# Kernel tuning notes

Measured on AMD Instinct MI355X. Metric: run time of the kernel, lower is better.

The kernel has to match this reference:

```python
import jax, jax.numpy as jnp
import numpy as np

N_POINTS = 262144
SP_FEAT = 128
HIDDEN = 64
EMBED = 256
NUM_SP = 4096
NUM_SP2 = 256
PAD_LIMIT = 64
MASK_RATIO = 0.6


def setup_inputs() -> dict:
    key = jax.random.key(0)
    ks = jax.random.split(key, 6)
    x = jax.random.normal(ks[0], (N_POINTS, SP_FEAT), jnp.float32)
    # point -> superpoint ids, sorted; force every superpoint non-empty
    idx10 = jax.random.randint(ks[1], (N_POINTS,), 0, NUM_SP)
    idx10 = jnp.sort(idx10.at[:NUM_SP].set(jnp.arange(NUM_SP))).astype(jnp.int32)
    # superpoint -> higher superpoint, balanced (16 per group, < PAD_LIMIT), sorted
    idx21 = ((jnp.arange(NUM_SP) * NUM_SP2) // NUM_SP).astype(jnp.int32)
    # deterministic mask: exactly int(NUM_SP * MASK_RATIO) superpoints masked
    mask_num = int(NUM_SP * MASK_RATIO)
    perm = jax.random.permutation(ks[2], NUM_SP)
    is_masked = jnp.zeros((NUM_SP,), bool).at[perm[:mask_num]].set(True)
    W1 = jax.random.normal(ks[3], (SP_FEAT, HIDDEN), jnp.float32) / np.sqrt(SP_FEAT).astype(np.float32)
    b1 = jnp.zeros((HIDDEN,), jnp.float32)
    W2 = jax.random.normal(ks[4], (HIDDEN, EMBED), jnp.float32) / np.sqrt(HIDDEN).astype(np.float32)
    b2 = jnp.zeros((EMBED,), jnp.float32)
    return {
        "full_features": x,
        "full_super_indices_10": idx10,
        "full_super_indices_21": idx21,
        "is_masked": is_masked,
        "W1": W1, "b1": b1, "W2": W2, "b2": b2,
    }


def _pad_scatter(tokens, idx21, flag):
    # tokens: [NUM_SP, C]; idx21 sorted sp->sp2 ids; flag: [NUM_SP] bool.
    # rank of each flagged superpoint within its sp2 group (in sp order)
    f = flag.astype(jnp.int32)
    cum = jnp.cumsum(f)                                            # inclusive global cumsum
    per_group = jax.ops.segment_sum(f, idx21, num_segments=NUM_SP2)
    prefix = jnp.concatenate([jnp.zeros((1,), jnp.int32), jnp.cumsum(per_group)[:-1]])
    rank = cum - 1 - prefix[idx21]                                 # 0-based slot within group
    slot = jnp.where(flag, rank, PAD_LIMIT)                        # PAD_LIMIT -> dropped
    out = jnp.zeros((NUM_SP2, PAD_LIMIT, tokens.shape[-1]), tokens.dtype)
    return out.at[idx21, slot].set(tokens, mode="drop")


def reference(full_features, full_super_indices_10, full_super_indices_21,
              is_masked, W1, b1, W2, b2):
    # per-point 2-layer MLP (gather is implicit: MLP is pointwise), then segment max
    h = jax.nn.relu(full_features @ W1 + b1)                       # [N, HIDDEN]
    h = jax.nn.relu(h @ W2 + b2)                                   # [N, EMBED]
    tok = jax.ops.segment_max(h, full_super_indices_10, num_segments=NUM_SP)  # [NUM_SP, EMBED]
    remain_tokens = _pad_scatter(tok, full_super_indices_21, ~is_masked)      # [NUM_SP2, PAD, EMBED]
    mask_tokens = _pad_scatter(tok, full_super_indices_21, is_masked)         # [NUM_SP2, PAD, EMBED]
    return (remain_tokens, mask_tokens)
```

## Files before the change

kernel.cpp:

```cpp
#include <hip/hip_runtime.h>
#include <hip/hip_bf16.h>

#define N_POINTS 262144
#define SP_FEAT 128
#define HIDDEN 64
#define EMBED 256
#define NUM_SP 4096
#define NUM_SP2 256
#define PAD_LIMIT 64
#define SLOTS 4
#define XS_STRIDE 136
#define H1_STRIDE 76
#define LOCAL_SP 4

typedef __bf16 bf16x8 __attribute__((ext_vector_type(8)));
typedef float floatx4 __attribute__((ext_vector_type(4)));
using bf16 = __hip_bfloat16;

__global__ __launch_bounds__(256) void fused_prep_kernel(
    const float* __restrict__ W1, const float* __restrict__ W2,
    const int* __restrict__ idx10, const int* __restrict__ idx21,
    const void* __restrict__ is_masked,
    bf16* __restrict__ W1t, bf16* __restrict__ W2t,
    int* __restrict__ start, int* __restrict__ invR, int* __restrict__ invM)
{
    const int tid = threadIdx.x;
    const int blk = blockIdx.x;

    if (blk < 256) {
        int p0 = (blk * 256 + tid) * 4;
        int4 v = *(const int4*)(idx10 + p0);
        if (p0 == 0) { start[0] = 0; start[NUM_SP] = N_POINTS; }
        if (v.y != v.x) start[v.y] = p0 + 1;
        if (v.z != v.y) start[v.z] = p0 + 2;
        if (v.w != v.z) start[v.w] = p0 + 3;
        if (p0 + 4 < N_POINTS) {
            int nx = idx10[p0 + 4];
            if (nx != v.w) start[nx] = p0 + 4;
        }
        return;
    }
    if (blk < 352) {
        int i = (blk - 256) * 256 + tid;
        if (i < HIDDEN * SP_FEAT) {
            int n = i >> 7, k = i & 127;
            W1t[i] = __float2bfloat16(W1[k * HIDDEN + n]);
        } else {
            int j = i - HIDDEN * SP_FEAT;
            int n = j >> 6, k = j & 63;
            W2t[j] = __float2bfloat16(W2[k * EMBED + n]);
        }
        return;
    }
    __shared__ int encS;
    if (tid == 0) encS = 0;
    __syncthreads();
    const unsigned char* mb = (const unsigned char*)is_masked;
    const int* mi = (const int*)is_masked;
    int local = 0;
    for (int p = tid; p < NUM_SP; p += 256)
        if ((p & 3) && mb[p]) local = 1;
    if (local) atomicOr(&encS, 1);
    __syncthreads();
    const int e = encS;

    const int g = tid;
    int a = 0, b = NUM_SP;
    while (a < b) { int m = (a + b) >> 1; if (idx21[m] < g) a = m + 1; else b = m; }
    int lo = a;
    b = NUM_SP;
    while (a < b) { int m = (a + b) >> 1; if (idx21[m] < g + 1) a = m + 1; else b = m; }
    int hi = a;
    int nR = 0, nM = 0;
    for (int s = lo; s < hi; ++s) {
        int msk = e ? (int)mb[s] : mi[s];
        if (msk) { if (nM < PAD_LIMIT) invM[g * PAD_LIMIT + nM] = s; nM++; }
        else     { if (nR < PAD_LIMIT) invR[g * PAD_LIMIT + nR] = s; nR++; }
    }
    for (int r = nR; r < PAD_LIMIT; ++r) invR[g * PAD_LIMIT + r] = -1;
    for (int r = nM; r < PAD_LIMIT; ++r) invM[g * PAD_LIMIT + r] = -1;
}

__global__ __launch_bounds__(256, 4) void mlp_segmax_kernel(
    const float* __restrict__ X, const int* __restrict__ idx10,
    const int* __restrict__ start,
    const bf16* __restrict__ W1t, const float* __restrict__ b1,
    const bf16* __restrict__ W2t, const float* __restrict__ b2,
    float* __restrict__ partial)
{
    __shared__ __align__(16) bf16 Xs[64][XS_STRIDE];
    __shared__ __align__(16) bf16 H1s[64][H1_STRIDE];
    __shared__ int tokL[LOCAL_SP][EMBED];
    __shared__ int sIdx[64];

    const int tid  = threadIdx.x;
    const int lane = tid & 63;
    const int w    = tid >> 6;
    const int l15  = lane & 15;
    const int quad = lane >> 4;
    const int b    = blockIdx.x;
    const int m0   = b * 64;

    float4 u0[4], u1[4];
#pragma unroll
    for (int i = 0; i < 4; ++i) {
        int c   = tid + 256 * i;
        int row = c >> 4;
        int cc  = (c & 15) * 8;
        const float* src = X + (size_t)(m0 + row) * SP_FEAT + cc;
        u0[i] = *(const float4*)src;
        u1[i] = *(const float4*)(src + 4);
    }
    if (tid < 64) sIdx[tid] = idx10[m0 + tid];
#pragma unroll
    for (int j = 0; j < LOCAL_SP; ++j) tokL[j][tid] = 0;

    bf16x8 bw1[4];
    {
        const bf16* p = W1t + (16 * w + l15) * SP_FEAT + quad * 8;
#pragma unroll
        for (int ks = 0; ks < 4; ++ks) bw1[ks] = *(const bf16x8*)(p + 32 * ks);
    }
    const float b1v = b1[16 * w + l15];

    __builtin_amdgcn_sched_barrier(0);

#pragma unroll
    for (int i = 0; i < 4; ++i) {
        int c   = tid + 256 * i;
        int row = c >> 4;
        int cc  = (c & 15) * 8;
        union { bf16x8 v; bf16 h[8]; } u;
        u.h[0] = __float2bfloat16(u0[i].x); u.h[1] = __float2bfloat16(u0[i].y);
        u.h[2] = __float2bfloat16(u0[i].z); u.h[3] = __float2bfloat16(u0[i].w);
        u.h[4] = __float2bfloat16(u1[i].x); u.h[5] = __float2bfloat16(u1[i].y);
        u.h[6] = __float2bfloat16(u1[i].z); u.h[7] = __float2bfloat16(u1[i].w);
        *(bf16x8*)(&Xs[row][cc]) = u.v;
    }
    __syncthreads();

    floatx4 zero4 = {0.f, 0.f, 0.f, 0.f};
    floatx4 acc1[4] = {zero4, zero4, zero4, zero4};
#pragma unroll
    for (int ks = 0; ks < 4; ++ks) {
        int k = ks * 32 + quad * 8;
#pragma unroll
        for (int tm = 0; tm < 4; ++tm) {
            bf16x8 a = *(bf16x8*)(&Xs[16 * tm + l15][k]);
            acc1[tm] = __builtin_amdgcn_mfma_f32_16x16x32_bf16(a, bw1[ks], acc1[tm], 0, 0, 0);
        }
    }
#pragma unroll
    for (int tm = 0; tm < 4; ++tm) {
#pragma unroll
        for (int r = 0; r < 4; ++r) {
            float v = acc1[tm][r] + b1v;
            v = v > 0.f ? v : 0.f;
            H1s[16 * tm + quad * 4 + r][16 * w + l15] = __float2bfloat16(v);
        }
    }
    __syncthreads();

    bf16x8 bf2[4][2];
#pragma unroll
    for (int tn = 0; tn < 4; ++tn) {
        const bf16* p = W2t + (64 * w + 16 * tn + l15) * HIDDEN + quad * 8;
#pragma unroll
        for (int ks = 0; ks < 2; ++ks) bf2[tn][ks] = *(const bf16x8*)(p + 32 * ks);
    }
    float b2f[4];
#pragma unroll
    for (int tn = 0; tn < 4; ++tn) b2f[tn] = b2[64 * w + 16 * tn + l15];

    bf16x8 afr[4][2];
    int sps[16];
#pragma unroll
    for (int tm = 0; tm < 4; ++tm) {
        afr[tm][0] = *(bf16x8*)(&H1s[16 * tm + l15][quad * 8]);
        afr[tm][1] = *(bf16x8*)(&H1s[16 * tm + l15][32 + quad * 8]);
        int4 s4 = *(const int4*)(&sIdx[16 * tm + 4 * quad]);
        sps[4 * tm + 0] = s4.x; sps[4 * tm + 1] = s4.y;
        sps[4 * tm + 2] = s4.z; sps[4 * tm + 3] = s4.w;
    }
    const int sp0 = sIdx[0];

#pragma unroll
    for (int tn = 0; tn < 4; ++tn) {
        const int col = 64 * w + 16 * tn + l15;
        int cur_sp = -1;
        float cur = 0.f;
#pragma unroll
        for (int tm = 0; tm < 4; ++tm) {
            floatx4 acc = zero4;
            acc = __builtin_amdgcn_mfma_f32_16x16x32_bf16(afr[tm][0], bf2[tn][0], acc, 0, 0, 0);
            acc = __builtin_amdgcn_mfma_f32_16x16x32_bf16(afr[tm][1], bf2[tn][1], acc, 0, 0, 0);
#pragma unroll
            for (int r = 0; r < 4; ++r) {
                float v = acc[r] + b2f[tn];
                v = v > 0.f ? v : 0.f;
                int sp = sps[4 * tm + r];
                if (sp == cur_sp) {
                    cur = fmaxf(cur, v);
                } else {
                    if (cur_sp >= 0) {
                        int local = cur_sp - sp0;
                        if (local < LOCAL_SP) {
                            atomicMax(&tokL[local][col], __float_as_int(cur));
                        } else {
                            int slot = b - (start[cur_sp] >> 6);
                            atomicMax((int*)(partial + ((size_t)cur_sp * SLOTS +
                                      (slot < 3 ? slot : 3)) * EMBED + col),
                                      __float_as_int(cur));
                        }
                    }
                    cur_sp = sp;
                    cur = v;
                }
            }
        }
        {
            int local = cur_sp - sp0;
            if (local < LOCAL_SP) {
                atomicMax(&tokL[local][col], __float_as_int(cur));
            } else {
                int slot = b - (start[cur_sp] >> 6);
                atomicMax((int*)(partial + ((size_t)cur_sp * SLOTS +
                          (slot < 3 ? slot : 3)) * EMBED + col),
                          __float_as_int(cur));
            }
        }
    }
    __syncthreads();

    int nsp = sIdx[63] - sp0 + 1;
    if (nsp > LOCAL_SP) nsp = LOCAL_SP;
    for (int j = 0; j < nsp; ++j) {
        int sp   = sp0 + j;
        int slot = b - (start[sp] >> 6);
        int bits = tokL[j][tid];
        int* dst = (int*)(partial + ((size_t)sp * SLOTS + (slot < 3 ? slot : 3)) * EMBED + tid);
        if (slot < 3) *dst = bits;
        else atomicMax(dst, bits);
    }
}

__global__ __launch_bounds__(256) void scatter_kernel(
    const float4* __restrict__ partial4, const int* __restrict__ start,
    const int* __restrict__ invR, const int* __restrict__ invM,
    float4* __restrict__ out4)
{
    const int bb   = blockIdx.x;
    const int g    = bb & (NUM_SP2 - 1);
    const int slab = bb >> 8;
    const int tid  = threadIdx.x;
    const int c4   = tid & 63;
    const int r0   = tid >> 6;
    const int* tab = slab ? invM : invR;
    float4* o = out4 + ((size_t)slab * NUM_SP2 + g) * PAD_LIMIT * 64;
#pragma unroll 4
    for (int rr = 0; rr < 16; ++rr) {
        int row = r0 + rr * 4;
        int sp = tab[g * PAD_LIMIT + row];
        float4 v = {0.f, 0.f, 0.f, 0.f};
        if (sp >= 0) {
            int sb = start[sp] >> 6;
            int se = (start[sp + 1] - 1) >> 6;
            int ns = se - sb;
            const float4* p = partial4 + (size_t)sp * SLOTS * 64 + c4;
            v = p[0];
            if (ns > 0) {
                float4 q = p[64];
                v.x = fmaxf(v.x, q.x); v.y = fmaxf(v.y, q.y);
                v.z = fmaxf(v.z, q.z); v.w = fmaxf(v.w, q.w);
            }
            if (ns > 1) {
                float4 q = p[128];
                v.x = fmaxf(v.x, q.x); v.y = fmaxf(v.y, q.y);
                v.z = fmaxf(v.z, q.z); v.w = fmaxf(v.w, q.w);
            }
            if (ns > 2) {
                float4 q = p[192];
                v.x = fmaxf(v.x, q.x); v.y = fmaxf(v.y, q.y);
                v.z = fmaxf(v.z, q.z); v.w = fmaxf(v.w, q.w);
            }
        }
        o[row * 64 + c4] = v;
    }
}

extern "C" void kernel_launch(void* const* d_in, const int* in_sizes, int n_in,
                              void* d_out, int out_size, void* d_ws, size_t ws_size,
                              hipStream_t stream) {
    (void)in_sizes; (void)n_in; (void)ws_size; (void)out_size;
    const float* X        = (const float*)d_in[0];
    const int* idx10      = (const int*)d_in[1];
    const int* idx21      = (const int*)d_in[2];
    const void* is_masked = (const void*)d_in[3];
    const float* W1       = (const float*)d_in[4];
    const float* b1       = (const float*)d_in[5];
    const float* W2       = (const float*)d_in[6];
    const float* b2       = (const float*)d_in[7];

    char* ws       = (char*)d_ws;
    float* partial = (float*)ws;
    bf16* W1t      = (bf16*)(ws + (size_t)NUM_SP * SLOTS * EMBED * 4);
    bf16* W2t      = W1t + HIDDEN * SP_FEAT;
    int*  start    = (int*)((char*)(W2t + EMBED * HIDDEN));
    int*  invR     = start + (NUM_SP + 2);
    int*  invM     = invR + NUM_SP2 * PAD_LIMIT;

    fused_prep_kernel<<<353, 256, 0, stream>>>(
        W1, W2, idx10, idx21, is_masked, W1t, W2t, start, invR, invM);
    mlp_segmax_kernel<<<N_POINTS / 64, 256, 0, stream>>>(
        X, idx10, start, W1t, b1, W2t, b2, partial);
    scatter_kernel<<<NUM_SP2 * 2, 256, 0, stream>>>(
        (const float4*)partial, start, invR, invM, (float4*)d_out);
}
```

Measured before the change: 251.0 us.

## Process four 64-row tiles per block with register prefetch of next tile

Each block of the MLP+segment-max kernel now loops over four consecutive 64-point tiles instead of one, with a quarter as many blocks. The next tile's X rows and superpoint indices are loaded into registers while the current tile's MFMAs run, overlapping global loads with compute and amortizing W2/bias loads. LOCAL_SP grows to 8 and the shared token buffer is flushed and cleared per tile, which adds syncs and shared memory. Fewer blocks (1024) may reduce latency hiding across the GPU.

```diff
diff --git a/kernel.cpp b/kernel.cpp
--- a/kernel.cpp
+++ b/kernel.cpp
@@ -9,9 +9,10 @@
 #define NUM_SP2 256
 #define PAD_LIMIT 64
 #define SLOTS 4
+#define TILES 4
 #define XS_STRIDE 136
 #define H1_STRIDE 76
-#define LOCAL_SP 4
+#define LOCAL_SP 8
 
 typedef __bf16 bf16x8 __attribute__((ext_vector_type(8)));
 typedef float floatx4 __attribute__((ext_vector_type(4)));
@@ -98,68 +99,26 @@
     const int w    = tid >> 6;
     const int l15  = lane & 15;
     const int quad = lane >> 4;
-    const int b    = blockIdx.x;
-    const int m0   = b * 64;
+    const int blk  = blockIdx.x;
+
+    const int srow = tid >> 4;
+    const int scc  = (tid & 15) * 8;
 
     float4 u0[4], u1[4];
-#pragma unroll
-    for (int i = 0; i < 4; ++i) {
-        int c   = tid + 256 * i;
-        int row = c >> 4;
-        int cc  = (c & 15) * 8;
-        const float* src = X + (size_t)(m0 + row) * SP_FEAT + cc;
-        u0[i] = *(const float4*)src;
-        u1[i] = *(const float4*)(src + 4);
-    }
-    if (tid < 64) sIdx[tid] = idx10[m0 + tid];
+    {
+        const float* src0 = X + (size_t)(blk * TILES * 64) * SP_FEAT;
+#pragma unroll
+        for (int i = 0; i < 4; ++i) {
+            const float* src = src0 + (size_t)(srow + 16 * i) * SP_FEAT + scc;
+            u0[i] = *(const float4*)src;
+            u1[i] = *(const float4*)(src + 4);
+        }
+    }
+    int i2 = 0;
+    if (tid < 64) i2 = idx10[blk * TILES * 64 + tid];
+
 #pragma unroll
     for (int j = 0; j < LOCAL_SP; ++j) tokL[j][tid] = 0;
-
-    bf16x8 bw1[4];
-    {
-        const bf16* p = W1t + (16 * w + l15) * SP_FEAT + quad * 8;
-#pragma unroll
-        for (int ks = 0; ks < 4; ++ks) bw1[ks] = *(const bf16x8*)(p + 32 * ks);
-    }
-    const float b1v = b1[16 * w + l15];
-
-    __builtin_amdgcn_sched_barrier(0);
-
-#pragma unroll
-    for (int i = 0; i < 4; ++i) {
-        int c   = tid + 256 * i;
-        int row = c >> 4;
-        int cc  = (c & 15) * 8;
-        union { bf16x8 v; bf16 h[8]; } u;
-        u.h[0] = __float2bfloat16(u0[i].x); u.h[1] = __float2bfloat16(u0[i].y);
-        u.h[2] = __float2bfloat16(u0[i].z); u.h[3] = __float2bfloat16(u0[i].w);
-        u.h[4] = __float2bfloat16(u1[i].x); u.h[5] = __float2bfloat16(u1[i].y);
-        u.h[6] = __float2bfloat16(u1[i].z); u.h[7] = __float2bfloat16(u1[i].w);
-        *(bf16x8*)(&Xs[row][cc]) = u.v;
-    }
-    __syncthreads();
-
-    floatx4 zero4 = {0.f, 0.f, 0.f, 0.f};
-    floatx4 acc1[4] = {zero4, zero4, zero4, zero4};
-#pragma unroll
-    for (int ks = 0; ks < 4; ++ks) {
-        int k = ks * 32 + quad * 8;
-#pragma unroll
-        for (int tm = 0; tm < 4; ++tm) {
-            bf16x8 a = *(bf16x8*)(&Xs[16 * tm + l15][k]);
-            acc1[tm] = __builtin_amdgcn_mfma_f32_16x16x32_bf16(a, bw1[ks], acc1[tm], 0, 0, 0);
-        }
-    }
-#pragma unroll
-    for (int tm = 0; tm < 4; ++tm) {
-#pragma unroll
-        for (int r = 0; r < 4; ++r) {
-            float v = acc1[tm][r] + b1v;
-            v = v > 0.f ? v : 0.f;
-            H1s[16 * tm + quad * 4 + r][16 * w + l15] = __float2bfloat16(v);
-        }
-    }
-    __syncthreads();
 
     bf16x8 bf2[4][2];
 #pragma unroll
@@ -171,76 +130,139 @@
     float b2f[4];
 #pragma unroll
     for (int tn = 0; tn < 4; ++tn) b2f[tn] = b2[64 * w + 16 * tn + l15];
-
-    bf16x8 afr[4][2];
-    int sps[16];
-#pragma unroll
-    for (int tm = 0; tm < 4; ++tm) {
-        afr[tm][0] = *(bf16x8*)(&H1s[16 * tm + l15][quad * 8]);
-        afr[tm][1] = *(bf16x8*)(&H1s[16 * tm + l15][32 + quad * 8]);
-        int4 s4 = *(const int4*)(&sIdx[16 * tm + 4 * quad]);
-        sps[4 * tm + 0] = s4.x; sps[4 * tm + 1] = s4.y;
-        sps[4 * tm + 2] = s4.z; sps[4 * tm + 3] = s4.w;
-    }
-    const int sp0 = sIdx[0];
-
-#pragma unroll
-    for (int tn = 0; tn < 4; ++tn) {
-        const int col = 64 * w + 16 * tn + l15;
-        int cur_sp = -1;
-        float cur = 0.f;
+    const float b1v = b1[16 * w + l15];
+
+    floatx4 zero4 = {0.f, 0.f, 0.f, 0.f};
+
+    for (int t = 0; t < TILES; ++t) {
+        const int bt = blk * TILES + t;
+        const int m0 = bt * 64;
+
+        if (tid < 64) sIdx[tid] = i2;
+
+        bf16x8 bw1[4];
+        {
+            const bf16* p = W1t + (16 * w + l15) * SP_FEAT + quad * 8;
+#pragma unroll
+            for (int ks = 0; ks < 4; ++ks) bw1[ks] = *(const bf16x8*)(p + 32 * ks);
+        }
+
+#pragma unroll
+        for (int i = 0; i < 4; ++i) {
+            union { bf16x8 v; bf16 h[8]; } u;
+            u.h[0] = __float2bfloat16(u0[i].x); u.h[1] = __float2bfloat16(u0[i].y);
+            u.h[2] = __float2bfloat16(u0[i].z); u.h[3] = __float2bfloat16(u0[i].w);
+            u.h[4] = __float2bfloat16(u1[i].x); u.h[5] = __float2bfloat16(u1[i].y);
+            u.h[6] = __float2bfloat16(u1[i].z); u.h[7] = __float2bfloat16(u1[i].w);
+            *(bf16x8*)(&Xs[srow + 16 * i][scc]) = u.v;
+        }
+        __syncthreads();
+
+        if (t + 1 < TILES) {
+            const float* src0 = X + (size_t)(m0 + 64) * SP_FEAT;
+#pragma unroll
+            for (int i = 0; i < 4; ++i) {
+                const float* src = src0 + (size_t)(srow + 16 * i) * SP_FEAT + scc;
+                u0[i] = *(const float4*)src;
+                u1[i] = *(const float4*)(src + 4);
+            }
+            if (tid < 64) i2 = idx10[m0 + 64 + tid];
+        }
+
+        floatx4 acc1[4] = {zero4, zero4, zero4, zero4};
+#pragma unroll
+        for (int ks = 0; ks < 4; ++ks) {
+            int k = ks * 32 + quad * 8;
+#pragma unroll
+            for (int tm = 0; tm < 4; ++tm) {
+                bf16x8 a = *(bf16x8*)(&Xs[16 * tm + l15][k]);
+                acc1[tm] = __builtin_amdgcn_mfma_f32_16x16x32_bf16(a, bw1[ks], acc1[tm], 0, 0, 0);
+            }
+        }
 #pragma unroll
         for (int tm = 0; tm < 4; ++tm) {
-            floatx4 acc = zero4;
-            acc = __builtin_amdgcn_mfma_f32_16x16x32_bf16(afr[tm][0], bf2[tn][0], acc, 0, 0, 0);
-            acc = __builtin_amdgcn_mfma_f32_16x16x32_bf16(afr[tm][1], bf2[tn][1], acc, 0, 0, 0);
 #pragma unroll
             for (int r = 0; r < 4; ++r) {
-                float v = acc[r] + b2f[tn];
+                float v = acc1[tm][r] + b1v;
                 v = v > 0.f ? v : 0.f;
-                int sp = sps[4 * tm + r];
-                if (sp == cur_sp) {
-                    cur = fmaxf(cur, v);
+                H1s[16 * tm + quad * 4 + r][16 * w + l15] = __float2bfloat16(v);
+            }
+        }
+        __syncthreads();
+
+        bf16x8 afr[4][2];
+        int sps[16];
+#pragma unroll
+        for (int tm = 0; tm < 4; ++tm) {
+            afr[tm][0] = *(bf16x8*)(&H1s[16 * tm + l15][quad * 8]);
+            afr[tm][1] = *(bf16x8*)(&H1s[16 * tm + l15][32 + quad * 8]);
+            int4 s4 = *(const int4*)(&sIdx[16 * tm + 4 * quad]);
+            sps[4 * tm + 0] = s4.x; sps[4 * tm + 1] = s4.y;
+            sps[4 * tm + 2] = s4.z; sps[4 * tm + 3] = s4.w;
+        }
+        const int sp0 = sIdx[0];
+
+#pragma unroll
+        for (int tn = 0; tn < 4; ++tn) {
+            const int col = 64 * w + 16 * tn + l15;
+            int cur_sp = -1;
+            float cur = 0.f;
+#pragma unroll
+            for (int tm = 0; tm < 4; ++tm) {
+                floatx4 acc = zero4;
+                acc = __builtin_amdgcn_mfma_f32_16x16x32_bf16(afr[tm][0], bf2[tn][0], acc, 0, 0, 0);
+                acc = __builtin_amdgcn_mfma_f32_16x16x32_bf16(afr[tm][1], bf2[tn][1], acc, 0, 0, 0);
+#pragma unroll
+                for (int r = 0; r < 4; ++r) {
+                    float v = acc[r] + b2f[tn];
+                    v = v > 0.f ? v : 0.f;
+                    int sp = sps[4 * tm + r];
+                    if (sp == cur_sp) {
+                        cur = fmaxf(cur, v);
+                    } else {
+                        if (cur_sp >= 0) {
+                            int local = cur_sp - sp0;
+                            if (local < LOCAL_SP) {
+                                atomicMax(&tokL[local][col], __float_as_int(cur));
+                            } else {
+                                int slot = bt - (start[cur_sp] >> 6);
+                                atomicMax((int*)(partial + ((size_t)cur_sp * SLOTS +
+                                          (slot < 3 ? slot : 3)) * EMBED + col),
+                                          __float_as_int(cur));
+                            }
+                        }
+                        cur_sp = sp;
+                        cur = v;
+                    }
+                }
+            }
+            {
+                int local = cur_sp - sp0;
+                if (local < LOCAL_SP) {
+                    atomicMax(&tokL[local][col], __float_as_int(cur));
                 } else {
-                    if (cur_sp >= 0) {
-                        int local = cur_sp - sp0;
-                        if (local < LOCAL_SP) {
-                            atomicMax(&tokL[local][col], __float_as_int(cur));
-                        } else {
-                            int slot = b - (start[cur_sp] >> 6);
-                            atomicMax((int*)(partial + ((size_t)cur_sp * SLOTS +
-                                      (slot < 3 ? slot : 3)) * EMBED + col),
-                                      __float_as_int(cur));
-                        }
-                    }
-                    cur_sp = sp;
-                    cur = v;
+                    int slot = bt - (start[cur_sp] >> 6);
+                    atomicMax((int*)(partial + ((size_t)cur_sp * SLOTS +
+                              (slot < 3 ? slot : 3)) * EMBED + col),
+                              __float_as_int(cur));
                 }
             }
         }
-        {
-            int local = cur_sp - sp0;
-            if (local < LOCAL_SP) {
-                atomicMax(&tokL[local][col], __float_as_int(cur));
-            } else {
-                int slot = b - (start[cur_sp] >> 6);
-                atomicMax((int*)(partial + ((size_t)cur_sp * SLOTS +
-                          (slot < 3 ? slot : 3)) * EMBED + col),
-                          __float_as_int(cur));
-            }
-        }
-    }
-    __syncthreads();
-
-    int nsp = sIdx[63] - sp0 + 1;
-    if (nsp > LOCAL_SP) nsp = LOCAL_SP;
-    for (int j = 0; j < nsp; ++j) {
-        int sp   = sp0 + j;
-        int slot = b - (start[sp] >> 6);
-        int bits = tokL[j][tid];
-        int* dst = (int*)(partial + ((size_t)sp * SLOTS + (slot < 3 ? slot : 3)) * EMBED + tid);
-        if (slot < 3) *dst = bits;
-        else atomicMax(dst, bits);
+        __syncthreads();
+
+        int nsp = sIdx[63] - sp0 + 1;
+        if (nsp > LOCAL_SP) nsp = LOCAL_SP;
+        for (int j = 0; j < nsp; ++j) {
+            int sp   = sp0 + j;
+            int slot = bt - (start[sp] >> 6);
+            int bits = tokL[j][tid];
+            int* dst = (int*)(partial + ((size_t)sp * SLOTS + (slot < 3 ? slot : 3)) * EMBED + tid);
+            if (slot < 3) *dst = bits;
+            else atomicMax(dst, bits);
+        }
+#pragma unroll
+        for (int j = 0; j < LOCAL_SP; ++j) tokL[j][tid] = 0;
+        __syncthreads();
     }
 }
 
@@ -311,7 +333,7 @@
 
     fused_prep_kernel<<<353, 256, 0, stream>>>(
         W1, W2, idx10, idx21, is_masked, W1t, W2t, start, invR, invM);
-    mlp_segmax_kernel<<<N_POINTS / 64, 256, 0, stream>>>(
+    mlp_segmax_kernel<<<N_POINTS / (64 * TILES), 256, 0, stream>>>(
         X, idx10, start, W1t, b1, W2t, b2, partial);
     scatter_kernel<<<NUM_SP2 * 2, 256, 0, stream>>>(
         (const float4*)partial, start, invR, invM, (float4*)d_out);
```

Result: slower. 288.2 us (+14.8%).
